# Kernel tuning notes

Measured on AMD Instinct MI355X. Metric: run time of the kernel, lower is better.

Reference implementation:

```python
import jax, jax.numpy as jnp
import numpy as np

H, W, S = 480, 1024, 32
MULT_THRESH, ADD_THRESH = 0.01, 0.1


def setup_inputs() -> dict:
    key = jax.random.key(0)
    k1, k2 = jax.random.split(key)
    flows_f = jax.random.normal(k1, (1, S, 2, H, W), jnp.float32)
    noise = jax.random.normal(k2, (1, S, 2, H, W), jnp.float32)
    # near-inverse backward flow so the fwd-bwd consistency check passes for many points
    flows_b = -flows_f + 0.05 * noise
    return {"flows_f": flows_f, "flows_b": flows_b, "margin": 10, "sample_step": 4}


def bilinear_sample(im, x, y):
    # im: (C,H,W); x,y: (N,) float pixel coords -> (C,N). Matches torch bilinear_sample2d
    # (weights from unclipped coords, gather indices clipped to the image).
    C, Hh, Ww = im.shape
    x0 = jnp.floor(x); y0 = jnp.floor(y)
    wx1 = x - x0; wx0 = 1.0 - wx1
    wy1 = y - y0; wy0 = 1.0 - wy1
    x0i = jnp.clip(x0.astype(jnp.int32), 0, Ww - 1)
    x1i = jnp.clip(x0i + 1, 0, Ww - 1)
    y0i = jnp.clip(y0.astype(jnp.int32), 0, Hh - 1)
    y1i = jnp.clip(y0i + 1, 0, Hh - 1)
    g = lambda yi, xi: im[:, yi, xi]  # (C,N)
    return (g(y0i, x0i) * (wy0 * wx0) + g(y0i, x1i) * (wy0 * wx1)
            + g(y1i, x0i) * (wy1 * wx0) + g(y1i, x1i) * (wy1 * wx1))


def _forward(ff, fb, margin, sample_step):
    # ff, fb: (S, 2, H, W) forward / backward flows (batch squeezed, B=1)
    gy = jnp.arange(margin, H - margin + 1, sample_step, dtype=jnp.float32)
    gx = jnp.arange(margin, W - margin + 1, sample_step, dtype=jnp.float32)
    YY, XX = jnp.meshgrid(gy, gx, indexing='ij')
    ys_g = YY.reshape(-1); xs_g = XX.reshape(-1)          # (G,) base sampling grid
    G = xs_g.shape[0]
    N = 2 * H * W // (sample_step ** 2)                   # trajectory slot capacity
    R = min(N, G)                                         # max births per step (static)

    by, bx = jnp.meshgrid(jnp.arange(H, dtype=jnp.float32),
                          jnp.arange(W, dtype=jnp.float32), indexing='ij')

    def prune(flow_f, flow_b):
        # fwd-bwd consistency mask 'on': (H,W) in {0,1}
        xt = (bx + flow_f[0]).reshape(-1)
        yt = (by + flow_f[1]).reshape(-1)
        fbw = bilinear_sample(flow_b, xt, yt).reshape(2, H, W)  # backwarped bwd flow
        diff = jnp.sqrt(jnp.sum((flow_f + fbw) ** 2, axis=0))
        mag = 0.5 * (jnp.sqrt(jnp.sum(flow_f ** 2, axis=0)) + jnp.sqrt(jnp.sum(fbw ** 2, axis=0)))
        return (diff <= MULT_THRESH * mag + ADD_THRESH).astype(jnp.float32)

    X = jnp.zeros((S, N), jnp.float32)
    Y = jnp.zeros((S, N), jnp.float32)
    Start = -jnp.ones((N,), jnp.float32)
    X = X.at[0, :G].set(xs_g)
    Y = Y.at[0, :G].set(ys_g)
    Start = Start.at[:G].set(0.0)

    def step(carry, inp):
        X, Y, Start = carry
        flow_f, flow_b, s = inp
        on = prune(flow_f, flow_b)                         # (H,W)
        active = Start >= 0.0                              # (N,) live-slot mask (replaces where(Start>=0))
        xs_o = X[s]; ys_o = Y[s]
        uv = bilinear_sample(flow_f, xs_o, ys_o)           # (2,N) flow at current points
        xs_t = xs_o + uv[0]; ys_t = ys_o + uv[1]
        fb_ok = bilinear_sample(on[None], xs_o, ys_o)[0] > 0.5
        marg = ((xs_t > margin) & (ys_t > margin) &
                (xs_t < W - margin) & (ys_t < H - margin))
        choose = active & marg & fb_ok
        # scatter surviving points into row s+1 (row starts as zeros, matching init)
        X = X.at[s + 1].set(jnp.where(choose, xs_t, 0.0))
        Y = Y.at[s + 1].set(jnp.where(choose, ys_t, 0.0))
        Start = jnp.where(active & ~choose, -1.0, Start)   # terminated slots freed
        # occupancy map of surviving targets, dilated by 5x5 ones-conv (== maxpool on binary)
        oy = jnp.where(choose, ys_t, jnp.float32(H)).astype(jnp.int32)
        ox = jnp.where(choose, xs_t, jnp.float32(W)).astype(jnp.int32)
        occ = jnp.zeros((H, W), jnp.float32).at[oy, ox].set(1.0, mode='drop')
        occ = jax.lax.reduce_window(occ, 0.0, jax.lax.max, (5, 5), (1, 1), 'SAME')
        map_occ = bilinear_sample(occ[None], xs_g, ys_g)[0]
        free_cand = (1.0 - map_occ) == 1.0                 # (G,) unoccupied grid points
        # compaction without dynamic shapes: stable-sort free-first, keep original order
        cand_order = jnp.argsort(~free_cand, stable=True)  # free candidates first
        num_cand = jnp.sum(free_cand)
        free_slot = Start < 0.0
        slot_order = jnp.argsort(~free_slot, stable=True)  # free slots first
        num_free = jnp.sum(free_slot)
        m = jnp.minimum(num_cand, num_free)
        r = jnp.arange(R)
        tgt = jnp.where(r < m, slot_order[:R], N)          # index N -> dropped
        X = X.at[s + 1, tgt].set(xs_g[cand_order[:R]], mode='drop')
        Y = Y.at[s + 1, tgt].set(ys_g[cand_order[:R]], mode='drop')
        Start = Start.at[tgt].set((s + 1).astype(jnp.float32), mode='drop')
        return (X, Y, Start), None

    steps = jnp.arange(S - 1)
    (X, Y, Start), _ = jax.lax.scan(step, (X, Y, Start), (ff[:-1], fb[:-1], steps))
    return jnp.stack([X, Y]), Start


def reference(flows_f, flows_b, margin, sample_step):
    # Returns dense trajectory buffers XY: (2, S, N) and final Start: (N,)
    # (the ragged python-list trajectory extraction is a host-side post-process).
    return _forward(flows_f[0], flows_b[0], margin, sample_step)
```

## Files before the change

kernel.cpp:

```cpp
#include <hip/hip_runtime.h>
#include <cstdint>

#define HH 480
#define WW 1024
#define SS 32
#define HW (HH*WW)
#define MARGIN 10
#define STEP 4
#define GYC 116
#define GXC 252
#define GG (GYC*GXC)
#define NSLOT (2*HH*WW/(STEP*STEP))
#define NBLK (NSLOT/256)
#define NWAVE (NSLOT/64)
#define CW ((GG+63)/64)
#define CWP 512
#define OCCB (CW*64)
#define FPW 256
#define CPB 122

__device__ __forceinline__ unsigned int aload(const unsigned int* p) {
  return __hip_atomic_load(p, __ATOMIC_RELAXED, __HIP_MEMORY_SCOPE_AGENT);
}
__device__ __forceinline__ void astore(unsigned int* p, unsigned int v) {
  __hip_atomic_store(p, v, __ATOMIC_RELAXED, __HIP_MEMORY_SCOPE_AGENT);
}
__device__ __forceinline__ unsigned long long aload64(const unsigned long long* p) {
  return __hip_atomic_load(p, __ATOMIC_RELAXED, __HIP_MEMORY_SCOPE_AGENT);
}
__device__ __forceinline__ void astore64(unsigned long long* p, unsigned long long v) {
  __hip_atomic_store(p, v, __ATOMIC_RELAXED, __HIP_MEMORY_SCOPE_AGENT);
}
__device__ __forceinline__ void astore8(unsigned char* p, unsigned char v) {
  __hip_atomic_store(p, v, __ATOMIC_RELAXED, __HIP_MEMORY_SCOPE_AGENT);
}

__device__ __forceinline__ int clampi(int v, int lo, int hi) {
  return v < lo ? lo : (v > hi ? hi : v);
}

__global__ __launch_bounds__(256) void k_init(unsigned long long* __restrict__ flags,
                                              unsigned int* __restrict__ occ32)
{
  int idx = blockIdx.x * 256 + threadIdx.x;
  if (idx < (2 * OCCB / 4)) occ32[idx] = 0u;
  if (idx < 256) {
    unsigned long long v = (idx < NBLK) ? 0ull : (0x7FFFFFFFull << 32);
    flags[idx] = v;
    flags[FPW + idx] = v;
  }
}

struct Bil {
  int x0i, x1i, y0i, y1i;
  int i00, i01, i10, i11;
  float w00, w01, w10, w11;
};

__device__ __forceinline__ Bil mkbil(float xs, float ys) {
#pragma clang fp contract(off)
  float x0 = floorf(xs), y0 = floorf(ys);
  float wx1 = xs - x0, wx0 = 1.0f - wx1;
  float wy1 = ys - y0, wy0 = 1.0f - wy1;
  Bil b;
  b.x0i = clampi((int)x0, 0, WW - 1);
  b.x1i = b.x0i + 1 > WW - 1 ? WW - 1 : b.x0i + 1;
  b.y0i = clampi((int)y0, 0, HH - 1);
  b.y1i = b.y0i + 1 > HH - 1 ? HH - 1 : b.y0i + 1;
  b.i00 = b.y0i * WW + b.x0i; b.i01 = b.y0i * WW + b.x1i;
  b.i10 = b.y1i * WW + b.x0i; b.i11 = b.y1i * WW + b.x1i;
  b.w00 = wy0 * wx0; b.w01 = wy0 * wx1;
  b.w10 = wy1 * wx0; b.w11 = wy1 * wx1;
  return b;
}

__device__ __forceinline__ float prune_val(float fx, float fy,
    float c00a, float c01a, float c10a, float c11a,
    float c00b, float c01b, float c10b, float c11b, const Bil& t)
{
#pragma clang fp contract(off)
  float bw0 = ((c00a * t.w00 + c01a * t.w01) + c10a * t.w10) + c11a * t.w11;
  float bw1 = ((c00b * t.w00 + c01b * t.w01) + c10b * t.w10) + c11b * t.w11;
  float t0 = fx + bw0, t1 = fy + bw1;
  float diff = sqrtf(t0 * t0 + t1 * t1);
  float magf = sqrtf(fx * fx + fy * fy);
  float magb = sqrtf(bw0 * bw0 + bw1 * bw1);
  float mag = 0.5f * (magf + magb);
  return (diff <= 0.01f * mag + 0.1f) ? 1.0f : 0.0f;
}

__device__ __forceinline__ unsigned long long make_intadv(
    int pix, int piy, float fx, float fy, const float* __restrict__ bks)
{
#pragma clang fp contract(off)
  float xt = (float)pix + fx, yt = (float)piy + fy;
  Bil Bt = mkbil(xt, yt);
  const float* b0p = bks;
  const float* b1p = bks + HW;
  float o = prune_val(fx, fy,
                      b0p[Bt.i00], b0p[Bt.i01], b0p[Bt.i10], b0p[Bt.i11],
                      b1p[Bt.i00], b1p[Bt.i01], b1p[Bt.i10], b1p[Bt.i11], Bt);
  bool marg = (xt > (float)MARGIN) && (yt > (float)MARGIN) &&
              (xt < (float)(WW - MARGIN)) && (yt < (float)(HH - MARGIN));
  bool ch = marg && (o > 0.5f);
  unsigned lo = __float_as_uint(ch ? xt : 0.0f);
  unsigned hi = __float_as_uint(ch ? yt : -1.0f);
  return ((unsigned long long)hi << 32) | (unsigned long long)lo;
}

__global__ __launch_bounds__(256, 1) void k_steps(
    const float* __restrict__ ff, const float* __restrict__ fbk,
    float* __restrict__ X, float* __restrict__ Y, float* __restrict__ Start,
    unsigned char* __restrict__ occ, unsigned long long* __restrict__ flags,
    unsigned long long* __restrict__ intadv)
{
#pragma clang fp contract(off)
  const int b = blockIdx.x;
  const int lane = threadIdx.x & 63;
  const int wv = threadIdx.x >> 6;
  const int slot = ((wv * NBLK + b) << 6) | lane;
  const unsigned long long ltmask = (1ull << lane) - 1ull;

  __shared__ unsigned long long wds[CWP];
  __shared__ unsigned int pref[CWP];
  __shared__ int wsum[4];
  __shared__ int wcnt[2][4];
  __shared__ int ps4[4];

  float x = 0.f, y = 0.f, st = -1.f;
  int mode = 0;
  float pf0 = 0.f, pf1 = 0.f, pf2 = 0.f, pf3 = 0.f;
  float pf4 = 0.f, pf5 = 0.f, pf6 = 0.f, pf7 = 0.f;
  float pb[32];
  float pxt = 0.f, pyt = 0.f;
  bool  pmarg = false;
  unsigned long long pa64 = (unsigned long long)0xBF800000u << 32;

  const int pj = threadIdx.x >> 1;
  const int pcell = b * CPB + pj;
  const bool prod = ((threadIdx.x & 1) == 0) && (pj < CPB) && (pcell < GG);
  int pix = 0, piy = 0, pp = 0;
  float fNx = 0.f, fNy = 0.f;
  float fCx = 0.f, fCy = 0.f;
  float bC0 = 0.f, bC1 = 0.f, bC2 = 0.f, bC3 = 0.f;
  float bC4 = 0.f, bC5 = 0.f, bC6 = 0.f, bC7 = 0.f;

  if (slot < GG) {
    int ii = slot / GXC, jj = slot - ii * GXC;
    int ix = MARGIN + STEP * jj, iy = MARGIN + STEP * ii;
    x = (float)ix; y = (float)iy;
    st = 0.f; mode = 2;
    int p0_ = iy * WW + ix;
    float f0x = ff[p0_], f0y = ff[HW + p0_];
    pa64 = make_intadv(ix, iy, f0x, f0y, fbk);
  }
  X[slot] = x; Y[slot] = y;

  if (prod) {
    int ii = pcell / GXC, jj = pcell - ii * GXC;
    pix = MARGIN + STEP * jj; piy = MARGIN + STEP * ii;
    pp = piy * WW + pix;
    float f1x = ff[(size_t)1 * 2 * HW + pp], f1y = ff[(size_t)1 * 2 * HW + HW + pp];
    float f2x = ff[(size_t)2 * 2 * HW + pp], f2y = ff[(size_t)2 * 2 * HW + HW + pp];
    float f3x = ff[(size_t)3 * 2 * HW + pp], f3y = ff[(size_t)3 * 2 * HW + HW + pp];
    fNx = ff[(size_t)4 * 2 * HW + pp];       fNy = ff[(size_t)4 * 2 * HW + HW + pp];
    astore64(&intadv[(size_t)1 * GG + pcell],
             make_intadv(pix, piy, f1x, f1y, fbk + (size_t)1 * 2 * HW));
    astore64(&intadv[(size_t)2 * GG + pcell],
             make_intadv(pix, piy, f2x, f2y, fbk + (size_t)2 * 2 * HW));
    {
      float xt = (float)pix + f3x, yt = (float)piy + f3y;
      Bil Bt = mkbil(xt, yt);
      const float* bb0 = fbk + (size_t)3 * 2 * HW;
      const float* bb1 = bb0 + HW;
      bC0 = bb0[Bt.i00]; bC1 = bb0[Bt.i01]; bC2 = bb0[Bt.i10]; bC3 = bb0[Bt.i11];
      bC4 = bb1[Bt.i00]; bC5 = bb1[Bt.i01]; bC6 = bb1[Bt.i10]; bC7 = bb1[Bt.i11];
      fCx = f3x; fCy = f3y;
    }
  }

#define ISSUE_TAP(tt, TXI, TYI, FX, FY) do { \
    Bil Bt = mkbil((float)P.TXI + (FX), (float)P.TYI + (FY)); \
    pb[(tt)*8+0] = b0n[Bt.i00]; pb[(tt)*8+1] = b0n[Bt.i01]; \
    pb[(tt)*8+2] = b0n[Bt.i10]; pb[(tt)*8+3] = b0n[Bt.i11]; \
    pb[(tt)*8+4] = b1n[Bt.i00]; pb[(tt)*8+5] = b1n[Bt.i01]; \
    pb[(tt)*8+6] = b1n[Bt.i10]; pb[(tt)*8+7] = b1n[Bt.i11]; \
  } while (0)

#define PRUNE_TAP(tt, TXI, TYI, FX, FY, OUT) do { \
    Bil Bt = mkbil((float)P.TXI + (FX), (float)P.TYI + (FY)); \
    OUT = prune_val((FX), (FY), \
                    pb[(tt)*8+0], pb[(tt)*8+1], pb[(tt)*8+2], pb[(tt)*8+3], \
                    pb[(tt)*8+4], pb[(tt)*8+5], pb[(tt)*8+6], pb[(tt)*8+7], Bt); \
  } while (0)

  for (int s = 0; s < SS - 1; ++s) {
    const unsigned char tag = (unsigned char)(s + 1);
    unsigned char* occw = occ + (((s + 1) & 1) ? OCCB : 0);

    bool moved = false;
    if (mode == 1) {
      Bil P = mkbil(x, y);
      float o0, o1, o2, o3;
      PRUNE_TAP(0, x0i, y0i, pf0, pf4, o0);
      PRUNE_TAP(1, x1i, y0i, pf1, pf5, o1);
      PRUNE_TAP(2, x0i, y1i, pf2, pf6, o2);
      PRUNE_TAP(3, x1i, y1i, pf3, pf7, o3);
      float fbv = ((o0 * P.w00 + o1 * P.w01) + o2 * P.w10) + o3 * P.w11;
      if (pmarg && fbv > 0.5f) {
        x = pxt; y = pyt;
        moved = true;
      } else { st = -1.f; x = 0.f; y = 0.f; mode = 0; }
    } else if (mode == 2) {
      float axt = __uint_as_float((unsigned)pa64);
      float ayt = __uint_as_float((unsigned)(pa64 >> 32));
      if (ayt >= 0.0f) {
        x = axt; y = ayt; mode = 1;
        moved = true;
      } else { st = -1.f; x = 0.f; y = 0.f; mode = 0; }
    }
    if (moved) {
      int oy = (int)y, ox = (int)x;
      int i0 = ((oy - (MARGIN + 2) + 4099) >> 2) - 1024;
      int i1 = ((oy - (MARGIN - 2) + 4096) >> 2) - 1024;
      int j0 = ((ox - (MARGIN + 2) + 4099) >> 2) - 1024;
      int j1 = ((ox - (MARGIN - 2) + 4096) >> 2) - 1024;
      if (i0 < 0) i0 = 0; if (i1 > GYC - 1) i1 = GYC - 1;
      if (j0 < 0) j0 = 0; if (j1 > GXC - 1) j1 = GXC - 1;
      for (int i = i0; i <= i1; ++i)
        for (int j = j0; j <= j1; ++j)
          astore8(&occw[i * GXC + j], tag);
    }
    unsigned long long smask = __ballot(st < 0.0f);
    if (lane == 0) wcnt[s & 1][wv] = (int)__popcll(smask);

    unsigned long long* fb = flags + (s & 1) * FPW;
    const int epoch = s + 1;
    __syncthreads();
    if (threadIdx.x == 0) {
      const int* wc = wcnt[s & 1];
      unsigned cpack = (unsigned)wc[0] | ((unsigned)wc[1] << 8)
                     | ((unsigned)wc[2] << 16) | ((unsigned)wc[3] << 24);
      astore64(&fb[b],
               ((unsigned long long)(unsigned)epoch << 32) | (unsigned long long)cpack);
    }

    if (mode == 1 && s < SS - 2) {
      const float* f0n = ff + (size_t)(s + 1) * 2 * HW;
      const float* f1n = f0n + HW;
      Bil P = mkbil(x, y);
      pf0 = f0n[P.i00]; pf1 = f0n[P.i01]; pf2 = f0n[P.i10]; pf3 = f0n[P.i11];
      pf4 = f1n[P.i00]; pf5 = f1n[P.i01]; pf6 = f1n[P.i10]; pf7 = f1n[P.i11];
      float u_ = ((pf0 * P.w00 + pf1 * P.w01) + pf2 * P.w10) + pf3 * P.w11;
      float v_ = ((pf4 * P.w00 + pf5 * P.w01) + pf6 * P.w10) + pf7 * P.w11;
      pxt = x + u_; pyt = y + v_;
      pmarg = (pxt > (float)MARGIN) && (pyt > (float)MARGIN) &&
              (pxt < (float)(WW - MARGIN)) && (pyt < (float)(HH - MARGIN));
      const float* b0n = fbk + (size_t)(s + 1) * 2 * HW;
      const float* b1n = b0n + HW;
      ISSUE_TAP(0, x0i, y0i, pf0, pf4);
      ISSUE_TAP(1, x1i, y0i, pf1, pf5);
      ISSUE_TAP(2, x0i, y1i, pf2, pf6);
      ISSUE_TAP(3, x1i, y1i, pf3, pf7);
    }
    if (prod) {
      if (s <= SS - 5) {
        float xt = (float)pix + fCx, yt = (float)piy + fCy;
        Bil Bt = mkbil(xt, yt);
        float o = prune_val(fCx, fCy, bC0, bC1, bC2, bC3, bC4, bC5, bC6, bC7, Bt);
        bool marg = (xt > (float)MARGIN) && (yt > (float)MARGIN) &&
                    (xt < (float)(WW - MARGIN)) && (yt < (float)(HH - MARGIN));
        bool ch = marg && (o > 0.5f);
        unsigned lo = __float_as_uint(ch ? xt : 0.0f);
        unsigned hi = __float_as_uint(ch ? yt : -1.0f);
        astore64(&intadv[(size_t)(s + 3) * GG + pcell],
                 ((unsigned long long)hi << 32) | (unsigned long long)lo);
      }
      if (s <= SS - 6) {
        float xt = (float)pix + fNx, yt = (float)piy + fNy;
        Bil Bt = mkbil(xt, yt);
        const float* bb0 = fbk + (size_t)(s + 4) * 2 * HW;
        const float* bb1 = bb0 + HW;
        bC0 = bb0[Bt.i00]; bC1 = bb0[Bt.i01]; bC2 = bb0[Bt.i10]; bC3 = bb0[Bt.i11];
        bC4 = bb1[Bt.i00]; bC5 = bb1[Bt.i01]; bC6 = bb1[Bt.i10]; bC7 = bb1[Bt.i11];
        fCx = fNx; fCy = fNy;
      }
      if (s <= SS - 7) {
        const float* fp_ = ff + (size_t)(s + 5) * 2 * HW;
        fNx = fp_[pp]; fNy = fp_[HW + pp];
      }
    }

    if (threadIdx.x < 64) {
      unsigned long long v0, v1, v2, v3;
      for (;;) {
        v0 = aload64(&fb[lane      ]);
        v1 = aload64(&fb[lane +  64]);
        v2 = aload64(&fb[lane + 128]);
        v3 = aload64(&fb[lane + 192]);
        unsigned m0 = (unsigned)(v0 >> 32), m1 = (unsigned)(v1 >> 32);
        unsigned m2 = (unsigned)(v2 >> 32), m3 = (unsigned)(v3 >> 32);
        unsigned mn = m0 < m1 ? m0 : m1;
        unsigned mn2 = m2 < m3 ? m2 : m3;
        mn = mn < mn2 ? mn : mn2;
        for (int o = 32; o > 0; o >>= 1) {
          unsigned t = (unsigned)__shfl_xor((int)mn, o, 64);
          mn = mn < t ? mn : t;
        }
        if ((int)mn >= epoch) break;
        __builtin_amdgcn_s_sleep(1);
      }
      auto up = [](unsigned long long f) -> unsigned long long {
        unsigned c = (unsigned)f;
        return (unsigned long long)(c & 0xFFu)
             | ((unsigned long long)((c >>  8) & 0xFFu) << 16)
             | ((unsigned long long)((c >> 16) & 0xFFu) << 32)
             | ((unsigned long long)((c >> 24) & 0xFFu) << 48);
      };
      unsigned long long u0 = up(v0), u1 = up(v1), u2 = up(v2), u3 = up(v3);
      unsigned long long F = u0 + u1 + u2 + u3;
      unsigned long long Pp = (lane       < b ? u0 : 0ull)
                            + (lane +  64 < b ? u1 : 0ull)
                            + (lane + 128 < b ? u2 : 0ull)
                            + (lane + 192 < b ? u3 : 0ull);
      for (int o = 32; o > 0; o >>= 1) {
        unsigned flo = (unsigned)F, fhi = (unsigned)(F >> 32);
        unsigned plo = (unsigned)Pp, phi = (unsigned)(Pp >> 32);
        unsigned flo2 = (unsigned)__shfl_xor((int)flo, o, 64);
        unsigned fhi2 = (unsigned)__shfl_xor((int)fhi, o, 64);
        unsigned plo2 = (unsigned)__shfl_xor((int)plo, o, 64);
        unsigned phi2 = (unsigned)__shfl_xor((int)phi, o, 64);
        F  += ((unsigned long long)fhi2 << 32) | flo2;
        Pp += ((unsigned long long)phi2 << 32) | plo2;
      }
      if (lane == 0) {
        int f0 = (int)(F & 0xFFFF), f1 = (int)((F >> 16) & 0xFFFF), f2 = (int)((F >> 32) & 0xFFFF);
        int p0 = (int)(Pp & 0xFFFF), p1 = (int)((Pp >> 16) & 0xFFFF);
        int p2 = (int)((Pp >> 32) & 0xFFFF), p3 = (int)((Pp >> 48) & 0xFFFF);
        ps4[0] = p0;
        ps4[1] = f0 + p1;
        ps4[2] = f0 + f1 + p2;
        ps4[3] = f0 + f1 + f2 + p3;
      }
    }
    __syncthreads();
    int ps = ps4[wv];

    unsigned long long cv[16];
    {
      const unsigned long long* occ64 =
          (const unsigned long long*)(occ + (((s + 1) & 1) ? OCCB : 0));
      int t = threadIdx.x;
#pragma unroll
      for (int r = 0; r < 16; ++r) {
        int j = t + 256 * r;
        cv[r] = (j < GG / 8) ? aload64(&occ64[j]) : 0ull;
      }
    }
    {
      unsigned char* nb = (unsigned char*)wds;
      const unsigned long long tr = 0x0101010101010101ull * (unsigned long long)tag;
      int t = threadIdx.x;
#pragma unroll
      for (int r = 0; r < 16; ++r) {
        int j = t + 256 * r;
        unsigned long long xx = cv[r] ^ tr;
        unsigned long long t1 = (xx & 0x7F7F7F7F7F7F7F7Full) + 0x7F7F7F7F7F7F7F7Full;
        unsigned long long nz = ((t1 | xx) >> 7) & 0x0101010101010101ull;
        unsigned char byte = (unsigned char)((nz * 0x0102040810204080ull) >> 56);
        nb[j] = (j < GG / 8) ? byte : (unsigned char)0;
      }
    }
    __syncthreads();
    {
      int t = threadIdx.x;
      int e0 = 2 * t, e1 = 2 * t + 1;
      unsigned long long m0 = wds[e0];
      unsigned long long m1 = wds[e1];
      int p0 = __popcll(m0), p1 = __popcll(m1);
      int v = p0 + p1;
      for (int o = 1; o < 64; o <<= 1) {
        int uu = __shfl_up(v, o, 64);
        if (lane >= o) v += uu;
      }
      if (lane == 63) wsum[wv] = v;
      __syncthreads();
      int base = 0;
      for (int j2 = 0; j2 < wv; ++j2) base += wsum[j2];
      pref[e0] = (unsigned int)(base + v - p1);
      pref[e1] = (unsigned int)(base + v);
      __syncthreads();
    }
    int tc = (int)pref[CWP - 1];

    if (st < 0.0f) {
      int r = ps + (int)__popcll(smask & ltmask);
      if (r < tc) {
        int k = 0;
        for (int bb = 256; bb >= 1; bb >>= 1) {
          int nk = k + bb;
          if (nk <= CWP - 1 && (int)pref[nk - 1] <= r) k = nk;
        }
        int j = r - (k ? (int)pref[k - 1] : 0);
        unsigned long long m = wds[k];
        int lo = 0;
        for (int bb = 32; bb >= 1; bb >>= 1) {
          int nb2 = lo + bb;
          unsigned long long mask = (nb2 >= 64) ? ~0ull : ((1ull << nb2) - 1ull);
          if (__popcll(m & mask) <= j) lo = nb2;
        }
        int g = k * 64 + lo;
        int ii = g / GXC, jj = g - ii * GXC;
        x = (float)(MARGIN + STEP * jj);
        y = (float)(MARGIN + STEP * ii);
        st = (float)(s + 1);
        mode = 2;
        if (s < SS - 2)
          pa64 = aload64(&intadv[(size_t)(s + 1) * GG + g]);
      }
    }
    X[(size_t)(s + 1) * NSLOT + slot] = x;
    Y[(size_t)(s + 1) * NSLOT + slot] = y;
  }

#undef ISSUE_TAP
#undef PRUNE_TAP

  Start[slot] = st;
}

extern "C" void kernel_launch(void* const* d_in, const int* in_sizes, int n_in,
                              void* d_out, int out_size, void* d_ws, size_t ws_size,
                              hipStream_t stream) {
  const float* ff  = (const float*)d_in[0];
  const float* fbk = (const float*)d_in[1];

  float* X     = (float*)d_out;
  float* Y     = X + (size_t)SS * NSLOT;
  float* Start = Y + (size_t)SS * NSLOT;

  unsigned long long* flags  = (unsigned long long*)d_ws;
  unsigned char*      occ    = (unsigned char*)(flags + 2 * FPW);
  unsigned long long* intadv = (unsigned long long*)(occ + 2 * OCCB);

  k_init<<<58, 256, 0, stream>>>(flags, (unsigned int*)occ);

  k_steps<<<NBLK, 256, 0, stream>>>(ff, fbk, X, Y, Start, occ, flags, intadv);
}
```

Measured before the change: 413.7 us.

## Replace byte occupancy map with per-step atomic-OR bitmaps and pair bilinear loads

The per-cell byte occupancy tags are replaced by a separate 64-bit-word bitmap for each step, set with atomic OR. Each step's free-cell scan now reads the bitmap words directly instead of loading bytes, comparing them to the tag and packing them into bits. Bilinear gathers also fetch horizontally adjacent pixels as one 8-byte load instead of two scalar loads. The atomic ORs can contend when many trajectories mark the same word, and the unaligned float2 loads rely on the hardware handling misaligned 8-byte accesses.

```diff
diff --git a/kernel.cpp b/kernel.cpp
--- a/kernel.cpp
+++ b/kernel.cpp
@@ -12,38 +12,39 @@
 #define GG (GYC*GXC)
 #define NSLOT (2*HH*WW/(STEP*STEP))
 #define NBLK (NSLOT/256)
-#define NWAVE (NSLOT/64)
 #define CW ((GG+63)/64)
 #define CWP 512
-#define OCCB (CW*64)
 #define FPW 256
 #define CPB 122
 
-__device__ __forceinline__ unsigned int aload(const unsigned int* p) {
-  return __hip_atomic_load(p, __ATOMIC_RELAXED, __HIP_MEMORY_SCOPE_AGENT);
-}
-__device__ __forceinline__ void astore(unsigned int* p, unsigned int v) {
-  __hip_atomic_store(p, v, __ATOMIC_RELAXED, __HIP_MEMORY_SCOPE_AGENT);
-}
 __device__ __forceinline__ unsigned long long aload64(const unsigned long long* p) {
   return __hip_atomic_load(p, __ATOMIC_RELAXED, __HIP_MEMORY_SCOPE_AGENT);
 }
 __device__ __forceinline__ void astore64(unsigned long long* p, unsigned long long v) {
   __hip_atomic_store(p, v, __ATOMIC_RELAXED, __HIP_MEMORY_SCOPE_AGENT);
 }
-__device__ __forceinline__ void astore8(unsigned char* p, unsigned char v) {
-  __hip_atomic_store(p, v, __ATOMIC_RELAXED, __HIP_MEMORY_SCOPE_AGENT);
+__device__ __forceinline__ void aor64(unsigned long long* p, unsigned long long v) {
+  (void)__hip_atomic_fetch_or(p, v, __ATOMIC_RELAXED, __HIP_MEMORY_SCOPE_AGENT);
 }
 
 __device__ __forceinline__ int clampi(int v, int lo, int hi) {
   return v < lo ? lo : (v > hi ? hi : v);
 }
 
+__device__ __forceinline__ void ld2(const float* __restrict__ base, int row, int xlo,
+                                    float& c0, float& c1) {
+  int bx = (xlo < WW - 1) ? xlo : (WW - 2);
+  float2 v;
+  __builtin_memcpy(&v, base + row * WW + bx, 8);
+  c0 = (xlo == bx) ? v.x : v.y;
+  c1 = v.y;
+}
+
 __global__ __launch_bounds__(256) void k_init(unsigned long long* __restrict__ flags,
-                                              unsigned int* __restrict__ occ32)
+                                              unsigned int* __restrict__ bmp32)
 {
   int idx = blockIdx.x * 256 + threadIdx.x;
-  if (idx < (2 * OCCB / 4)) occ32[idx] = 0u;
+  if (idx < 32 * CWP * 2) bmp32[idx] = 0u;
   if (idx < 256) {
     unsigned long long v = (idx < NBLK) ? 0ull : (0x7FFFFFFFull << 32);
     flags[idx] = v;
@@ -111,7 +112,7 @@
 __global__ __launch_bounds__(256, 1) void k_steps(
     const float* __restrict__ ff, const float* __restrict__ fbk,
     float* __restrict__ X, float* __restrict__ Y, float* __restrict__ Start,
-    unsigned char* __restrict__ occ, unsigned long long* __restrict__ flags,
+    unsigned long long* __restrict__ bmp, unsigned long long* __restrict__ flags,
     unsigned long long* __restrict__ intadv)
 {
 #pragma clang fp contract(off)
@@ -173,18 +174,20 @@
       Bil Bt = mkbil(xt, yt);
       const float* bb0 = fbk + (size_t)3 * 2 * HW;
       const float* bb1 = bb0 + HW;
-      bC0 = bb0[Bt.i00]; bC1 = bb0[Bt.i01]; bC2 = bb0[Bt.i10]; bC3 = bb0[Bt.i11];
-      bC4 = bb1[Bt.i00]; bC5 = bb1[Bt.i01]; bC6 = bb1[Bt.i10]; bC7 = bb1[Bt.i11];
+      ld2(bb0, Bt.y0i, Bt.x0i, bC0, bC1);
+      ld2(bb0, Bt.y1i, Bt.x0i, bC2, bC3);
+      ld2(bb1, Bt.y0i, Bt.x0i, bC4, bC5);
+      ld2(bb1, Bt.y1i, Bt.x0i, bC6, bC7);
       fCx = f3x; fCy = f3y;
     }
   }
 
 #define ISSUE_TAP(tt, TXI, TYI, FX, FY) do { \
     Bil Bt = mkbil((float)P.TXI + (FX), (float)P.TYI + (FY)); \
-    pb[(tt)*8+0] = b0n[Bt.i00]; pb[(tt)*8+1] = b0n[Bt.i01]; \
-    pb[(tt)*8+2] = b0n[Bt.i10]; pb[(tt)*8+3] = b0n[Bt.i11]; \
-    pb[(tt)*8+4] = b1n[Bt.i00]; pb[(tt)*8+5] = b1n[Bt.i01]; \
-    pb[(tt)*8+6] = b1n[Bt.i10]; pb[(tt)*8+7] = b1n[Bt.i11]; \
+    ld2(b0n, Bt.y0i, Bt.x0i, pb[(tt)*8+0], pb[(tt)*8+1]); \
+    ld2(b0n, Bt.y1i, Bt.x0i, pb[(tt)*8+2], pb[(tt)*8+3]); \
+    ld2(b1n, Bt.y0i, Bt.x0i, pb[(tt)*8+4], pb[(tt)*8+5]); \
+    ld2(b1n, Bt.y1i, Bt.x0i, pb[(tt)*8+6], pb[(tt)*8+7]); \
   } while (0)
 
 #define PRUNE_TAP(tt, TXI, TYI, FX, FY, OUT) do { \
@@ -195,8 +198,7 @@
   } while (0)
 
   for (int s = 0; s < SS - 1; ++s) {
-    const unsigned char tag = (unsigned char)(s + 1);
-    unsigned char* occw = occ + (((s + 1) & 1) ? OCCB : 0);
+    unsigned long long* pl = bmp + (size_t)(s + 1) * CWP;
 
     bool moved = false;
     if (mode == 1) {
@@ -227,9 +229,13 @@
       int j1 = ((ox - (MARGIN - 2) + 4096) >> 2) - 1024;
       if (i0 < 0) i0 = 0; if (i1 > GYC - 1) i1 = GYC - 1;
       if (j0 < 0) j0 = 0; if (j1 > GXC - 1) j1 = GXC - 1;
-      for (int i = i0; i <= i1; ++i)
-        for (int j = j0; j <= j1; ++j)
-          astore8(&occw[i * GXC + j], tag);
+      for (int i = i0; i <= i1; ++i) {
+        int g0 = i * GXC + j0;
+        int w = g0 >> 6, bo = g0 & 63;
+        unsigned long long m = ((j1 > j0) ? 3ull : 1ull) << bo;
+        aor64(&pl[w], m);
+        if (bo == 63 && j1 > j0) aor64(&pl[w + 1], 1ull);
+      }
     }
     unsigned long long smask = __ballot(st < 0.0f);
     if (lane == 0) wcnt[s & 1][wv] = (int)__popcll(smask);
@@ -249,8 +255,10 @@
       const float* f0n = ff + (size_t)(s + 1) * 2 * HW;
       const float* f1n = f0n + HW;
       Bil P = mkbil(x, y);
-      pf0 = f0n[P.i00]; pf1 = f0n[P.i01]; pf2 = f0n[P.i10]; pf3 = f0n[P.i11];
-      pf4 = f1n[P.i00]; pf5 = f1n[P.i01]; pf6 = f1n[P.i10]; pf7 = f1n[P.i11];
+      ld2(f0n, P.y0i, P.x0i, pf0, pf1);
+      ld2(f0n, P.y1i, P.x0i, pf2, pf3);
+      ld2(f1n, P.y0i, P.x0i, pf4, pf5);
+      ld2(f1n, P.y1i, P.x0i, pf6, pf7);
       float u_ = ((pf0 * P.w00 + pf1 * P.w01) + pf2 * P.w10) + pf3 * P.w11;
       float v_ = ((pf4 * P.w00 + pf5 * P.w01) + pf6 * P.w10) + pf7 * P.w11;
       pxt = x + u_; pyt = y + v_;
@@ -281,8 +289,10 @@
         Bil Bt = mkbil(xt, yt);
         const float* bb0 = fbk + (size_t)(s + 4) * 2 * HW;
         const float* bb1 = bb0 + HW;
-        bC0 = bb0[Bt.i00]; bC1 = bb0[Bt.i01]; bC2 = bb0[Bt.i10]; bC3 = bb0[Bt.i11];
-        bC4 = bb1[Bt.i00]; bC5 = bb1[Bt.i01]; bC6 = bb1[Bt.i10]; bC7 = bb1[Bt.i11];
+        ld2(bb0, Bt.y0i, Bt.x0i, bC0, bC1);
+        ld2(bb0, Bt.y1i, Bt.x0i, bC2, bC3);
+        ld2(bb1, Bt.y0i, Bt.x0i, bC4, bC5);
+        ld2(bb1, Bt.y1i, Bt.x0i, bC6, bC7);
         fCx = fNx; fCy = fNy;
       }
       if (s <= SS - 7) {
@@ -346,37 +356,15 @@
     __syncthreads();
     int ps = ps4[wv];
 
-    unsigned long long cv[16];
-    {
-      const unsigned long long* occ64 =
-          (const unsigned long long*)(occ + (((s + 1) & 1) ? OCCB : 0));
-      int t = threadIdx.x;
-#pragma unroll
-      for (int r = 0; r < 16; ++r) {
-        int j = t + 256 * r;
-        cv[r] = (j < GG / 8) ? aload64(&occ64[j]) : 0ull;
-      }
-    }
-    {
-      unsigned char* nb = (unsigned char*)wds;
-      const unsigned long long tr = 0x0101010101010101ull * (unsigned long long)tag;
-      int t = threadIdx.x;
-#pragma unroll
-      for (int r = 0; r < 16; ++r) {
-        int j = t + 256 * r;
-        unsigned long long xx = cv[r] ^ tr;
-        unsigned long long t1 = (xx & 0x7F7F7F7F7F7F7F7Full) + 0x7F7F7F7F7F7F7F7Full;
-        unsigned long long nz = ((t1 | xx) >> 7) & 0x0101010101010101ull;
-        unsigned char byte = (unsigned char)((nz * 0x0102040810204080ull) >> 56);
-        nb[j] = (j < GG / 8) ? byte : (unsigned char)0;
-      }
-    }
-    __syncthreads();
     {
       int t = threadIdx.x;
       int e0 = 2 * t, e1 = 2 * t + 1;
-      unsigned long long m0 = wds[e0];
-      unsigned long long m1 = wds[e1];
+      unsigned long long m0 = 0ull, m1 = 0ull;
+      if (e0 < CW) m0 = ~aload64(&pl[e0]);
+      if (e1 < CW) m1 = ~aload64(&pl[e1]);
+      if (e0 == CW - 1) m0 &= (1ull << 48) - 1ull;
+      if (e1 == CW - 1) m1 &= (1ull << 48) - 1ull;
+      wds[e0] = m0; wds[e1] = m1;
       int p0 = __popcll(m0), p1 = __popcll(m1);
       int v = p0 + p1;
       for (int o = 1; o < 64; o <<= 1) {
@@ -440,10 +428,10 @@
   float* Start = Y + (size_t)SS * NSLOT;
 
   unsigned long long* flags  = (unsigned long long*)d_ws;
-  unsigned char*      occ    = (unsigned char*)(flags + 2 * FPW);
-  unsigned long long* intadv = (unsigned long long*)(occ + 2 * OCCB);
-
-  k_init<<<58, 256, 0, stream>>>(flags, (unsigned int*)occ);
-
-  k_steps<<<NBLK, 256, 0, stream>>>(ff, fbk, X, Y, Start, occ, flags, intadv);
-}
+  unsigned long long* bmp    = flags + 2 * FPW;
+  unsigned long long* intadv = bmp + 32 * CWP;
+
+  k_init<<<128, 256, 0, stream>>>(flags, (unsigned int*)bmp);
+
+  k_steps<<<NBLK, 256, 0, stream>>>(ff, fbk, X, Y, Start, bmp, flags, intadv);
+}
```

Measured after the change: 385.4 us. -6.8%, faster.
